# Kernel tuning notes

Measured on AMD Instinct MI355X. Metric: run time of the kernel, lower is better.

The kernel has to match this reference:

```python
import jax, jax.numpy as jnp
import numpy as np

CLASSES = 5

def setup_inputs() -> dict:
    key = jax.random.key(0)
    k1, k2, k3, k4 = jax.random.split(key, 4)
    B, C, H, Wd = 4, 128, 256, 256
    MS = 8
    image = jax.random.normal(k1, (B, C, H, Wd), dtype=jnp.float32)
    clusters = jax.random.randint(k2, (B, 1, H, Wd), 0, CLASSES, dtype=jnp.int64)
    # nn.Linear-style init: U(-1/sqrt(fan_in), 1/sqrt(fan_in))
    bound = 1.0 / np.sqrt(C)
    W = jax.random.uniform(k3, (CLASSES, MS, C), minval=-bound, maxval=bound, dtype=jnp.float32)
    b = jax.random.uniform(k4, (CLASSES, MS), minval=-bound, maxval=bound, dtype=jnp.float32)
    return {"image": image, "clusters": clusters, "W": W, "b": b}

def reference(image, clusters, W, b):
    # image: [B, C, H, W]; clusters: [B, 1, H, W] with labels in [0, CLASSES)
    # Per-pixel: out = relu(x @ W_l^T + b_l) where l = cluster label of that pixel.
    x = jnp.transpose(image, (0, 2, 3, 1))              # [B, H, W, C]
    # Dense per-class linear + relu: [B, H, W, L, M]
    all_out = jax.nn.relu(jnp.einsum('bhwc,lmc->bhwlm', x, W) + b)
    labels = clusters[:, 0]                              # [B, H, W]
    sel = jnp.take_along_axis(all_out, labels[..., None, None], axis=3)[..., 0, :]  # [B,H,W,M]
    # Pixels with label >= CLASSES would remain zero in the original; randint keeps all in range.
    valid = (labels >= 0) & (labels < CLASSES)
    sel = jnp.where(valid[..., None], sel, 0.0)
    return jnp.transpose(sel, (0, 3, 1, 2))              # [B, M, H, W]
```

## Files before the change

kernel.cpp:

```cpp
#include <hip/hip_runtime.h>

#define NCLASSES 5
#define MS 8
#define NC 128
#define HW (256 * 256)
#define BLK 512

__global__ __launch_bounds__(BLK, 4) void clusterdown_kernel(
    const float* __restrict__ image,
    const int* __restrict__ clusters,
    const float* __restrict__ Wg,
    const float* __restrict__ bg,
    float* __restrict__ out,
    int n_pix)
{
    __shared__ float wlds[NC * NCLASSES * MS];
    __shared__ float blds[NCLASSES * MS];

    const int tid = threadIdx.x;

    for (int j = tid; j < (NCLASSES * MS * NC) / 4; j += BLK) {
        const float4 w4 = ((const float4*)Wg)[j];
        const int i = j * 4;
        const int l = i >> 10;
        const int m = (i >> 7) & (MS - 1);
        const int c = i & (NC - 1);
        wlds[((c + 0) * NCLASSES + l) * MS + m] = w4.x;
        wlds[((c + 1) * NCLASSES + l) * MS + m] = w4.y;
        wlds[((c + 2) * NCLASSES + l) * MS + m] = w4.z;
        wlds[((c + 3) * NCLASSES + l) * MS + m] = w4.w;
    }
    if (tid < NCLASSES * MS) blds[tid] = bg[tid];
    __syncthreads();

    const int p = blockIdx.x * BLK + tid;
    if (p >= n_pix) return;

    const int bidx = p / HW;
    const int hw   = p - bidx * HW;

    const int lab = clusters[p];
    const bool valid = (lab >= 0) && (lab < NCLASSES);
    const int l = valid ? lab : 0;

    float acc[MS];
#pragma unroll
    for (int m = 0; m < MS; ++m) acc[m] = blds[l * MS + m];

    const float* ip = image + (size_t)bidx * NC * HW + hw;

#pragma unroll 16
    for (int c = 0; c < NC; ++c) {
        const float v = ip[(size_t)c * HW];
        const float4* wp = (const float4*)&wlds[(c * NCLASSES + l) * MS];
        const float4 w0 = wp[0];
        const float4 w1 = wp[1];
        acc[0] = fmaf(v, w0.x, acc[0]);
        acc[1] = fmaf(v, w0.y, acc[1]);
        acc[2] = fmaf(v, w0.z, acc[2]);
        acc[3] = fmaf(v, w0.w, acc[3]);
        acc[4] = fmaf(v, w1.x, acc[4]);
        acc[5] = fmaf(v, w1.y, acc[5]);
        acc[6] = fmaf(v, w1.z, acc[6]);
        acc[7] = fmaf(v, w1.w, acc[7]);
    }

    float* op = out + (size_t)bidx * MS * HW + hw;
#pragma unroll
    for (int m = 0; m < MS; ++m) {
        const float r = valid ? fmaxf(acc[m], 0.0f) : 0.0f;
        op[(size_t)m * HW] = r;
    }
}

extern "C" void kernel_launch(void* const* d_in, const int* in_sizes, int n_in,
                              void* d_out, int out_size, void* d_ws, size_t ws_size,
                              hipStream_t stream) {
    const float* image  = (const float*)d_in[0];
    const int* clusters = (const int*)d_in[1];
    const float* Wg     = (const float*)d_in[2];
    const float* bg     = (const float*)d_in[3];
    float* out          = (float*)d_out;

    const int n_pix = in_sizes[1];
    const int grid  = (n_pix + BLK - 1) / BLK;

    clusterdown_kernel<<<grid, BLK, 0, stream>>>(image, clusters, Wg, bg, out, n_pix);
}
```

Measured before the change: 30.30 us.

## Use nontemporal loads/stores, halve block size, restructure weight staging and channel loop

Halves the block size to 256 threads and replaces the float4 weight-transpose staging with a scalar loop that reads the weights transposed into LDS. It uses nontemporal loads for the image and cluster labels and nontemporal stores for the output, since this streaming data is never reused. The channel loop now loads 8 channel values up front before their FMAs, with the outer loop not unrolled, to group memory requests. It also swaps the divide and modulo for shift and mask. Smaller blocks mean more blocks, and each one repeats the per-block weight staging.

```diff
diff --git a/kernel.cpp b/kernel.cpp
--- a/kernel.cpp
+++ b/kernel.cpp
@@ -4,7 +4,7 @@
 #define MS 8
 #define NC 128
 #define HW (256 * 256)
-#define BLK 512
+#define BLK 256
 
 __global__ __launch_bounds__(BLK, 4) void clusterdown_kernel(
     const float* __restrict__ image,
@@ -19,16 +19,10 @@
 
     const int tid = threadIdx.x;
 
-    for (int j = tid; j < (NCLASSES * MS * NC) / 4; j += BLK) {
-        const float4 w4 = ((const float4*)Wg)[j];
-        const int i = j * 4;
-        const int l = i >> 10;
-        const int m = (i >> 7) & (MS - 1);
-        const int c = i & (NC - 1);
-        wlds[((c + 0) * NCLASSES + l) * MS + m] = w4.x;
-        wlds[((c + 1) * NCLASSES + l) * MS + m] = w4.y;
-        wlds[((c + 2) * NCLASSES + l) * MS + m] = w4.z;
-        wlds[((c + 3) * NCLASSES + l) * MS + m] = w4.w;
+    for (int k = tid; k < NC * NCLASSES * MS; k += BLK) {
+        const int c  = k / (NCLASSES * MS);
+        const int lm = k - c * (NCLASSES * MS);
+        wlds[k] = Wg[lm * NC + c];
     }
     if (tid < NCLASSES * MS) blds[tid] = bg[tid];
     __syncthreads();
@@ -36,10 +30,10 @@
     const int p = blockIdx.x * BLK + tid;
     if (p >= n_pix) return;
 
-    const int bidx = p / HW;
-    const int hw   = p - bidx * HW;
+    const int bidx = p >> 16;
+    const int hw   = p & (HW - 1);
 
-    const int lab = clusters[p];
+    const int lab = __builtin_nontemporal_load(&clusters[p]);
     const bool valid = (lab >= 0) && (lab < NCLASSES);
     const int l = valid ? lab : 0;
 
@@ -49,27 +43,33 @@
 
     const float* ip = image + (size_t)bidx * NC * HW + hw;
 
-#pragma unroll 16
-    for (int c = 0; c < NC; ++c) {
-        const float v = ip[(size_t)c * HW];
-        const float4* wp = (const float4*)&wlds[(c * NCLASSES + l) * MS];
-        const float4 w0 = wp[0];
-        const float4 w1 = wp[1];
-        acc[0] = fmaf(v, w0.x, acc[0]);
-        acc[1] = fmaf(v, w0.y, acc[1]);
-        acc[2] = fmaf(v, w0.z, acc[2]);
-        acc[3] = fmaf(v, w0.w, acc[3]);
-        acc[4] = fmaf(v, w1.x, acc[4]);
-        acc[5] = fmaf(v, w1.y, acc[5]);
-        acc[6] = fmaf(v, w1.z, acc[6]);
-        acc[7] = fmaf(v, w1.w, acc[7]);
+#pragma unroll 1
+    for (int cc = 0; cc < NC; cc += 8) {
+        float v[8];
+#pragma unroll
+        for (int k = 0; k < 8; ++k)
+            v[k] = __builtin_nontemporal_load(&ip[(size_t)(cc + k) * HW]);
+#pragma unroll
+        for (int k = 0; k < 8; ++k) {
+            const float4* wp = (const float4*)&wlds[((cc + k) * NCLASSES + l) * MS];
+            const float4 w0 = wp[0];
+            const float4 w1 = wp[1];
+            acc[0] = fmaf(v[k], w0.x, acc[0]);
+            acc[1] = fmaf(v[k], w0.y, acc[1]);
+            acc[2] = fmaf(v[k], w0.z, acc[2]);
+            acc[3] = fmaf(v[k], w0.w, acc[3]);
+            acc[4] = fmaf(v[k], w1.x, acc[4]);
+            acc[5] = fmaf(v[k], w1.y, acc[5]);
+            acc[6] = fmaf(v[k], w1.z, acc[6]);
+            acc[7] = fmaf(v[k], w1.w, acc[7]);
+        }
     }
 
     float* op = out + (size_t)bidx * MS * HW + hw;
 #pragma unroll
     for (int m = 0; m < MS; ++m) {
         const float r = valid ? fmaxf(acc[m], 0.0f) : 0.0f;
-        op[(size_t)m * HW] = r;
+        __builtin_nontemporal_store(r, &op[(size_t)m * HW]);
     }
 }
 
```

New measurement: 35.31 us. 1.17x slower.
